# Optimization experiments

Measured on AMD Instinct MI355X. Metric: run time of the kernel, lower is better.

Reference implementation:

```python
import jax, jax.numpy as jnp
import numpy as np

NUM_IMUS = 13
NUM_PARAMS = 9
EPS = 1e-5
LN_EPS = 1e-5


def setup_inputs() -> dict:
    key = jax.random.key(0)
    k1, k2, k3 = jax.random.split(key, 3)
    d_model, S = 512, 2048
    hidden_states = jax.random.normal(k1, (1, S, d_model), dtype=jnp.float32)
    min_orig_accel_norm = jax.random.normal(k2, (1,), dtype=jnp.float32)
    W = jax.random.normal(k3, (d_model, NUM_IMUS * NUM_PARAMS), dtype=jnp.float32) * 0.02
    b = jnp.zeros((NUM_IMUS * NUM_PARAMS,), jnp.float32)
    ln_w = jnp.ones((d_model,), jnp.float32)
    ln_b = jnp.zeros((d_model,), jnp.float32)
    return {"hidden_states": hidden_states, "min_orig_accel_norm": min_orig_accel_norm,
            "ln_w": ln_w, "ln_b": ln_b, "W": W, "b": b}


def _layernorm(x, w, bias):
    mu = x.mean(-1, keepdims=True)
    var = ((x - mu) ** 2).mean(-1, keepdims=True)
    return (x - mu) * jax.lax.rsqrt(var + LN_EPS) * w + bias


def reference(hidden_states, min_orig_accel_norm, ln_w, ln_b, W, b):
    S = hidden_states.shape[1]
    x = _layernorm(hidden_states, ln_w, ln_b)
    # (1,S,117) -> (S, 9, 13); batch is always 1
    p = (x @ W + b).reshape(S, NUM_PARAMS, NUM_IMUS)
    c, c_th, phi, phi_th = p[:, 4], p[:, 5], p[:, 6], p[:, 7]  # (S,13) each
    d = jnp.sqrt(p[:, 1] ** 2 + EPS)                 # (S,13)
    k = d ** 2 / 4 + jax.nn.softplus(p[:, 0])
    d_th = jnp.sqrt(p[:, 3] ** 2 + EPS)
    k_th = d_th ** 2 / 4 + jax.nn.softplus(p[:, 2])
    noise_bias = p[:, 8].T                           # (13,S)
    om = jnp.sqrt(4 * k - d ** 2) / 2                # = sqrt(softplus(p0))
    om_th = jnp.sqrt(4 * k_th - d_th ** 2) / 2
    t = jnp.arange(S, dtype=jnp.float32)
    tstep = jnp.triu(t[None, :] - t[:, None])        # (S,S), entry (i,j)=j-i for j>=i
    ts = tstep[:, :, None]                           # (S,S,1)

    def src(a):  # params indexed by source step i, broadcast over target step j
        return a[:, None, :]                         # (S,1,13)

    lin = src(c) * jnp.exp(-src(d) / 2 * ts) * jnp.sin(ts * src(om) + src(phi))
    ang = src(c_th) * jnp.exp(-src(d_th) / 2 * ts) * jnp.sin(ts * src(om_th) + src(phi_th))
    mask = jnp.triu(jnp.ones((S, S), jnp.float32))[:, :, None]
    summed = ((lin + ang) * mask).sum(axis=0)        # (S,13): sum over source i<=j
    return summed.T + min_orig_accel_norm + noise_bias  # (13,S)
```

## Files before the change

### kernel.cpp

```cpp
#include <hip/hip_runtime.h>
#include <math.h>

#define S_LEN 2048
#define D_MODEL 512
#define NIMU 13
#define NCOL 117
#define CPAD 128
#define NKC 8
#define KCSTRIDE ((size_t)CPAD * S_LEN)

static __device__ __forceinline__ float softplus_f(float x) {
    return (x > 20.f) ? x : log1pf(expf(x));
}

static __device__ __forceinline__ void osc_init(float pk, float pd, float amp, float phi, float dtf,
                                                float& re, float& im, float& zr, float& zi)
{
    const float LOG2E = 1.4426950408889634f;
    const float INV2PI = 0.15915494309189535f;
    float d = sqrtf(pd * pd + 1e-5f);
    float kk = d * d * 0.25f + softplus_f(pk);
    float om = 0.5f * sqrtf(fmaxf(4.f * kk - d * d, 0.f));
    float y = -0.5f * d * LOG2E;
    float f = om * INV2PI;
    float ph = phi * INV2PI;
    float ez = __builtin_amdgcn_exp2f(y);
    zr = ez * __builtin_amdgcn_cosf(f);
    zi = ez * __builtin_amdgcn_sinf(f);
    float er = amp * __builtin_amdgcn_exp2f(dtf * y);
    float r = fmaf(dtf, f, ph); r -= floorf(r);
    re = er * __builtin_amdgcn_cosf(r);
    im = er * __builtin_amdgcn_sinf(r);
}

__global__ __launch_bounds__(256) void stats_kernel(const float* __restrict__ H,
                                                    float2* __restrict__ stats,
                                                    const float* __restrict__ W,
                                                    float* __restrict__ Wp,
                                                    float* __restrict__ out) {
    if (blockIdx.x < 104) out[blockIdx.x * 256 + threadIdx.x] = 0.f;
    if (threadIdx.x < CPAD) {
        int c = threadIdx.x;
        Wp[blockIdx.x * CPAD + c] = (c < NCOL) ? W[blockIdx.x * NCOL + c] : 0.f;
    }
    int wave = threadIdx.x >> 6;
    int lane = threadIdx.x & 63;
    int row = blockIdx.x * 4 + wave;
    const float* hr = H + row * D_MODEL;
    float4 a = *(const float4*)&hr[lane * 4];
    float4 b = *(const float4*)&hr[256 + lane * 4];
    float sum = a.x + a.y + a.z + a.w + b.x + b.y + b.z + b.w;
    #pragma unroll
    for (int off = 32; off; off >>= 1) sum += __shfl_down(sum, off);
    sum = __shfl(sum, 0);
    float mu = sum * (1.f / 512.f);
    float vs = 0.f;
    vs += (a.x - mu) * (a.x - mu); vs += (a.y - mu) * (a.y - mu);
    vs += (a.z - mu) * (a.z - mu); vs += (a.w - mu) * (a.w - mu);
    vs += (b.x - mu) * (b.x - mu); vs += (b.y - mu) * (b.y - mu);
    vs += (b.z - mu) * (b.z - mu); vs += (b.w - mu) * (b.w - mu);
    #pragma unroll
    for (int off = 32; off; off >>= 1) vs += __shfl_down(vs, off);
    if (lane == 0) {
        float var = vs * (1.f / 512.f);
        stats[row] = make_float2(mu, 1.0f / sqrtf(var + 1e-5f));
    }
}

__global__ __launch_bounds__(128) void proj_kernel(
    const float* __restrict__ H, const float2* __restrict__ stats,
    const float* __restrict__ lnw, const float* __restrict__ lnb,
    const float* __restrict__ Wp, float* __restrict__ Pt)
{
    __shared__ float Xt[64 * 32];
    __shared__ float Ws[64 * CPAD];
    int tid = threadIdx.x;
    int row0 = blockIdx.x * 32;
    int k0 = blockIdx.y * 64;

    {
        const float4* Wp4 = (const float4*)(Wp + k0 * CPAD);
        float4* Ws4 = (float4*)Ws;
        #pragma unroll
        for (int i = 0; i < 16; ++i) Ws4[tid + i * 128] = Wp4[tid + i * 128];
    }
    {
        int r = tid >> 2, fq = tid & 3;
        int row = row0 + r;
        float2 st = stats[row];
        const float4* H4 = (const float4*)(H + row * D_MODEL + k0);
        const float4* w4 = (const float4*)(lnw + k0);
        const float4* b4 = (const float4*)(lnb + k0);
        #pragma unroll
        for (int it = 0; it < 4; ++it) {
            int q = fq + it * 4;
            float4 h = H4[q], wv = w4[q], bv = b4[q];
            Xt[(4 * q + 0) * 32 + r] = (h.x - st.x) * st.y * wv.x + bv.x;
            Xt[(4 * q + 1) * 32 + r] = (h.y - st.x) * st.y * wv.y + bv.y;
            Xt[(4 * q + 2) * 32 + r] = (h.z - st.x) * st.y * wv.z + bv.z;
            Xt[(4 * q + 3) * 32 + r] = (h.w - st.x) * st.y * wv.w + bv.w;
        }
    }
    __syncthreads();

    int q8 = tid & 15;
    int rg = tid >> 4;
    float acc[4][8];
    #pragma unroll
    for (int a = 0; a < 4; ++a)
        for (int u = 0; u < 8; ++u) acc[a][u] = 0.f;

    #pragma unroll 4
    for (int k = 0; k < 64; ++k) {
        float4 xa = *(float4*)&Xt[k * 32 + 4 * rg];
        float4 w0 = *(float4*)&Ws[k * CPAD + 8 * q8];
        float4 w1 = *(float4*)&Ws[k * CPAD + 8 * q8 + 4];
        float xv[4] = {xa.x, xa.y, xa.z, xa.w};
        float wv[8] = {w0.x, w0.y, w0.z, w0.w, w1.x, w1.y, w1.z, w1.w};
        #pragma unroll
        for (int a = 0; a < 4; ++a)
            #pragma unroll
            for (int u = 0; u < 8; ++u)
                acc[a][u] = fmaf(xv[a], wv[u], acc[a][u]);
    }

    if (q8 < 15) {
        #pragma unroll
        for (int u = 0; u < 8; ++u) {
            int c = 8 * q8 + u;
            if (c < NCOL) {
                float4 v = make_float4(acc[0][u], acc[1][u], acc[2][u], acc[3][u]);
                *(float4*)&Pt[((size_t)blockIdx.y * CPAD + c) * S_LEN + row0 + 4 * rg] = v;
            }
        }
    }
}

__global__ __launch_bounds__(256) void main_kernel(
    const float* __restrict__ Pt, const float* __restrict__ bias,
    const float* __restrict__ minp, float* __restrict__ out)
{
    __shared__ float buf[4 * 256];
    int tid = threadIdx.x;
    int lane = tid & 63, w = tid >> 6;
    int m = blockIdx.y;
    int bx = blockIdx.x;

    int g = 0, base = 0;
    #pragma unroll 1
    for (;;) {
        int nb = (g + 4) >> 2;
        if (bx < base + nb) break;
        base += nb; ++g;
    }
    int sub = bx - base;
    int q = sub * 4 + w;

    float* accW = buf + w * 256;
    accW[lane] = 0.f; accW[lane + 64] = 0.f;
    accW[lane + 128] = 0.f; accW[lane + 192] = 0.f;
    __builtin_amdgcn_wave_barrier();

    if (q <= g) {
        int sc = q, tc = g - q;
        int i0 = sc * 128;
        float dtf = (float)(tc * 128);

        float pvA[9], pvB[9];
        #pragma unroll
        for (int p = 0; p < 9; ++p) {
            int c = p * 13 + m;
            const float* bp = Pt + (size_t)c * S_LEN + i0 + lane;
            float vA = bias[c], vB = vA;
            #pragma unroll
            for (int kc = 0; kc < NKC; ++kc) {
                vA += bp[kc * KCSTRIDE];
                vB += bp[kc * KCSTRIDE + 64];
            }
            pvA[p] = vA; pvB[p] = vB;
        }

        float reLA, imLA, zrLA, ziLA; osc_init(pvA[0], pvA[1], pvA[4], pvA[6], dtf, reLA, imLA, zrLA, ziLA);
        float reAA, imAA, zrAA, ziAA; osc_init(pvA[2], pvA[3], pvA[5], pvA[7], dtf, reAA, imAA, zrAA, ziAA);
        float reLB, imLB, zrLB, ziLB; osc_init(pvB[0], pvB[1], pvB[4], pvB[6], dtf, reLB, imLB, zrLB, ziLB);
        float reAB, imAB, zrAB, ziAB; osc_init(pvB[2], pvB[3], pvB[5], pvB[7], dtf, reAB, imAB, zrAB, ziAB);

        #pragma unroll 8
        for (int t = 0; t < 128; ++t) {
            float a0 = accW[lane + t];
            float a1 = accW[lane + 64 + t];
            a0 += imLA + imAA;
            a1 += imLB + imAB;
            accW[lane + t] = a0;
            accW[lane + 64 + t] = a1;
            __builtin_amdgcn_wave_barrier();
            float tL = imLA * ziLA; float rL = fmaf(reLA, zrLA, -tL);
            imLA = fmaf(reLA, ziLA, imLA * zrLA); reLA = rL;
            float tA = imAA * ziAA; float rA = fmaf(reAA, zrAA, -tA);
            imAA = fmaf(reAA, ziAA, imAA * zrAA); reAA = rA;
            float tLB = imLB * ziLB; float rLB = fmaf(reLB, zrLB, -tLB);
            imLB = fmaf(reLB, ziLB, imLB * zrLB); reLB = rLB;
            float tAB = imAB * ziAB; float rAB = fmaf(reAB, zrAB, -tAB);
            imAB = fmaf(reAB, ziAB, imAB * zrAB); reAB = rAB;
        }
    }
    __syncthreads();

    {
        int j = g * 128 + tid;
        if (j < S_LEN) {
            float s = buf[tid] + buf[256 + tid] + buf[512 + tid] + buf[768 + tid];
            if (sub == 0 && tid < 128) {
                int c8 = 8 * 13 + m;
                float v = minp[0] + bias[c8];
                const float* bp = Pt + (size_t)c8 * S_LEN + j;
                #pragma unroll
                for (int kc = 0; kc < NKC; ++kc) v += bp[kc * KCSTRIDE];
                s += v;
            }
            atomicAdd(&out[m * S_LEN + j], s);
        }
    }
}

extern "C" void kernel_launch(void* const* d_in, const int* in_sizes, int n_in,
                              void* d_out, int out_size, void* d_ws, size_t ws_size,
                              hipStream_t stream)
{
    const float* H    = (const float*)d_in[0];
    const float* MINP = (const float*)d_in[1];
    const float* LNW  = (const float*)d_in[2];
    const float* LNB  = (const float*)d_in[3];
    const float* W    = (const float*)d_in[4];
    const float* B    = (const float*)d_in[5];
    float* out = (float*)d_out;

    const size_t PTSZ = (size_t)NKC * CPAD * S_LEN * sizeof(float);
    const size_t STSZ = S_LEN * sizeof(float2);

    char* ws = (char*)d_ws;
    float*  Pt    = (float*)ws;
    float2* stats = (float2*)(ws + PTSZ);
    float*  Wp    = (float*)(ws + PTSZ + STSZ);

    stats_kernel<<<512, 256, 0, stream>>>(H, stats, W, Wp, out);
    proj_kernel<<<dim3(64, 8), 128, 0, stream>>>(H, stats, LNW, LNB, Wp, Pt);
    main_kernel<<<dim3(40, NIMU), 256, 0, stream>>>(Pt, B, MINP, out);
}
```

Before: 98.98 us.

## Pre-reduce split-K projection and use 64-step oscillator tiles with register carry

Adds a separate reduce kernel that sums the eight split-K partial projections plus bias once into a compact buffer, instead of having every main-kernel wave re-sum them. The main kernel moves from 128-step tiles with two oscillator sets per lane to 64-step tiles with one set per lane. That launches more blocks (144 instead of 40 per IMU) to improve occupancy and load balance. The running sum is now carried in a register, with one shared-memory read and one write per step instead of two of each. The cost is an extra kernel launch, more atomics, and a workspace buffer placed after Wp.

```diff
diff --git a/kernel.cpp b/kernel.cpp
--- a/kernel.cpp
+++ b/kernel.cpp
@@ -136,11 +136,28 @@
     }
 }
 
+__global__ __launch_bounds__(256) void reduce_kernel(const float* __restrict__ Pt,
+                                                     const float* __restrict__ bias,
+                                                     float* __restrict__ Pred)
+{
+    int c = blockIdx.y;
+    int s4 = blockIdx.x * 256 + threadIdx.x;
+    const float4* p4 = (const float4*)(Pt + (size_t)c * S_LEN) + s4;
+    float b = bias[c];
+    float4 acc = make_float4(b, b, b, b);
+    #pragma unroll
+    for (int kc = 0; kc < NKC; ++kc) {
+        float4 v = p4[kc * (KCSTRIDE / 4)];
+        acc.x += v.x; acc.y += v.y; acc.z += v.z; acc.w += v.w;
+    }
+    ((float4*)(Pred + (size_t)c * S_LEN))[s4] = acc;
+}
+
 __global__ __launch_bounds__(256) void main_kernel(
-    const float* __restrict__ Pt, const float* __restrict__ bias,
+    const float* __restrict__ Pred,
     const float* __restrict__ minp, float* __restrict__ out)
 {
-    __shared__ float buf[4 * 256];
+    __shared__ float buf[4 * 128];
     int tid = threadIdx.x;
     int lane = tid & 63, w = tid >> 6;
     int m = blockIdx.y;
@@ -156,67 +173,45 @@
     int sub = bx - base;
     int q = sub * 4 + w;
 
-    float* accW = buf + w * 256;
+    float* accW = buf + w * 128;
     accW[lane] = 0.f; accW[lane + 64] = 0.f;
-    accW[lane + 128] = 0.f; accW[lane + 192] = 0.f;
     __builtin_amdgcn_wave_barrier();
 
     if (q <= g) {
         int sc = q, tc = g - q;
-        int i0 = sc * 128;
-        float dtf = (float)(tc * 128);
-
-        float pvA[9], pvB[9];
-        #pragma unroll
-        for (int p = 0; p < 9; ++p) {
-            int c = p * 13 + m;
-            const float* bp = Pt + (size_t)c * S_LEN + i0 + lane;
-            float vA = bias[c], vB = vA;
-            #pragma unroll
-            for (int kc = 0; kc < NKC; ++kc) {
-                vA += bp[kc * KCSTRIDE];
-                vB += bp[kc * KCSTRIDE + 64];
-            }
-            pvA[p] = vA; pvB[p] = vB;
-        }
-
-        float reLA, imLA, zrLA, ziLA; osc_init(pvA[0], pvA[1], pvA[4], pvA[6], dtf, reLA, imLA, zrLA, ziLA);
-        float reAA, imAA, zrAA, ziAA; osc_init(pvA[2], pvA[3], pvA[5], pvA[7], dtf, reAA, imAA, zrAA, ziAA);
-        float reLB, imLB, zrLB, ziLB; osc_init(pvB[0], pvB[1], pvB[4], pvB[6], dtf, reLB, imLB, zrLB, ziLB);
-        float reAB, imAB, zrAB, ziAB; osc_init(pvB[2], pvB[3], pvB[5], pvB[7], dtf, reAB, imAB, zrAB, ziAB);
-
+        int i0 = sc * 64;
+        float dtf = (float)(tc * 64);
+
+        float pv[9];
+        #pragma unroll
+        for (int p = 0; p < 9; ++p)
+            pv[p] = Pred[(size_t)(p * 13 + m) * S_LEN + i0 + lane];
+
+        float reL, imL, zrL, ziL; osc_init(pv[0], pv[1], pv[4], pv[6], dtf, reL, imL, zrL, ziL);
+        float reA, imA, zrA, ziA; osc_init(pv[2], pv[3], pv[5], pv[7], dtf, reA, imA, zrA, ziA);
+
+        float a = 0.f;
         #pragma unroll 8
-        for (int t = 0; t < 128; ++t) {
-            float a0 = accW[lane + t];
-            float a1 = accW[lane + 64 + t];
-            a0 += imLA + imAA;
-            a1 += imLB + imAB;
-            accW[lane + t] = a0;
-            accW[lane + 64 + t] = a1;
+        for (int t = 0; t < 64; ++t) {
+            a += imL + imA;
+            accW[lane + t] = a;
             __builtin_amdgcn_wave_barrier();
-            float tL = imLA * ziLA; float rL = fmaf(reLA, zrLA, -tL);
-            imLA = fmaf(reLA, ziLA, imLA * zrLA); reLA = rL;
-            float tA = imAA * ziAA; float rA = fmaf(reAA, zrAA, -tA);
-            imAA = fmaf(reAA, ziAA, imAA * zrAA); reAA = rA;
-            float tLB = imLB * ziLB; float rLB = fmaf(reLB, zrLB, -tLB);
-            imLB = fmaf(reLB, ziLB, imLB * zrLB); reLB = rLB;
-            float tAB = imAB * ziAB; float rAB = fmaf(reAB, zrAB, -tAB);
-            imAB = fmaf(reAB, ziAB, imAB * zrAB); reAB = rAB;
+            float nxt = accW[lane + t + 1];
+            float tL = imL * ziL; float rL = fmaf(reL, zrL, -tL);
+            imL = fmaf(reL, ziL, imL * zrL); reL = rL;
+            float tA = imA * ziA; float rA = fmaf(reA, zrA, -tA);
+            imA = fmaf(reA, ziA, imA * zrA); reA = rA;
+            a = nxt;
         }
     }
     __syncthreads();
 
-    {
-        int j = g * 128 + tid;
+    if (tid < 128) {
+        int j = g * 64 + tid;
         if (j < S_LEN) {
-            float s = buf[tid] + buf[256 + tid] + buf[512 + tid] + buf[768 + tid];
-            if (sub == 0 && tid < 128) {
-                int c8 = 8 * 13 + m;
-                float v = minp[0] + bias[c8];
-                const float* bp = Pt + (size_t)c8 * S_LEN + j;
-                #pragma unroll
-                for (int kc = 0; kc < NKC; ++kc) v += bp[kc * KCSTRIDE];
-                s += v;
+            float s = buf[tid] + buf[128 + tid] + buf[256 + tid] + buf[384 + tid];
+            if (sub == 0 && tid < 64) {
+                s += minp[0] + Pred[(size_t)(8 * 13 + m) * S_LEN + j];
             }
             atomicAdd(&out[m * S_LEN + j], s);
         }
@@ -237,13 +232,16 @@
 
     const size_t PTSZ = (size_t)NKC * CPAD * S_LEN * sizeof(float);
     const size_t STSZ = S_LEN * sizeof(float2);
+    const size_t WPSZ = (size_t)D_MODEL * CPAD * sizeof(float);
 
     char* ws = (char*)d_ws;
     float*  Pt    = (float*)ws;
     float2* stats = (float2*)(ws + PTSZ);
     float*  Wp    = (float*)(ws + PTSZ + STSZ);
+    float*  Pred  = (float*)(ws + PTSZ + STSZ + WPSZ);
 
     stats_kernel<<<512, 256, 0, stream>>>(H, stats, W, Wp, out);
     proj_kernel<<<dim3(64, 8), 128, 0, stream>>>(H, stats, LNW, LNB, Wp, Pt);
-    main_kernel<<<dim3(40, NIMU), 256, 0, stream>>>(Pt, B, MINP, out);
-}
+    reduce_kernel<<<dim3(2, NCOL), 256, 0, stream>>>(Pt, B, Pred);
+    main_kernel<<<dim3(144, NIMU), 256, 0, stream>>>(Pred, MINP, out);
+}
```

After: 92.04 us (median of 2 runs). 1.08x faster.
